# Kernel tuning notes

Measured on AMD Instinct MI355X. Metric: run time of the kernel, lower is better.

Reference implementation:

```python
import jax, jax.numpy as jnp
import numpy as np
import math

D_MODEL, N_HEADS, D_K, D_C, D_HR = 1024, 8, 128, 32, 32
B, S = 4, 2048


def setup_inputs() -> dict:
    key = jax.random.key(0)
    ks = jax.random.split(key, 17)
    def lin(k, fan_in, fan_out):
        lim = 1.0 / math.sqrt(fan_in)
        kw, kb = jax.random.split(k)
        W = jax.random.uniform(kw, (fan_in, fan_out), jnp.float32, -lim, lim)
        b = jax.random.uniform(kb, (fan_out,), jnp.float32, -lim, lim)
        return W, b
    W_DQ, b_DQ = lin(ks[0], D_MODEL, D_C)
    W_UQ, b_UQ = lin(ks[1], D_C, N_HEADS * D_K)
    W_DKV, b_DKV = lin(ks[2], D_MODEL, D_C)
    W_UK, b_UK = lin(ks[3], D_C, N_HEADS * D_K)
    W_UV, b_UV = lin(ks[4], D_C, N_HEADS * D_K)
    W_QR, b_QR = lin(ks[5], D_C, N_HEADS * D_HR)
    W_KR, b_KR = lin(ks[6], D_MODEL, D_HR)
    W_O, b_O = lin(ks[7], N_HEADS * D_K, D_MODEL)
    h_t = jax.random.normal(ks[8], (B, S, D_MODEL), jnp.float32)
    return {"h_t": h_t,
            "W_DQ": W_DQ, "b_DQ": b_DQ, "W_UQ": W_UQ, "b_UQ": b_UQ,
            "W_DKV": W_DKV, "b_DKV": b_DKV, "W_UK": W_UK, "b_UK": b_UK,
            "W_UV": W_UV, "b_UV": b_UV, "W_QR": W_QR, "b_QR": b_QR,
            "W_KR": W_KR, "b_KR": b_KR, "W_O": W_O, "b_O": b_O}


def reference(h_t, W_DQ, b_DQ, W_UQ, b_UQ, W_DKV, b_DKV, W_UK, b_UK,
              W_UV, b_UV, W_QR, b_QR, W_KR, b_KR, W_O, b_O):
    b, s, _ = h_t.shape
    # low-rank latent projections
    c_q = h_t @ W_DQ + b_DQ                       # [B,S,d_c]
    c_kv = h_t @ W_DKV + b_DKV                    # [B,S,d_c]
    # content heads: [B,H,S,d_k]
    q_c = (c_q @ W_UQ + b_UQ).reshape(b, s, N_HEADS, D_K).transpose(0, 2, 1, 3)
    k_c = (c_kv @ W_UK + b_UK).reshape(b, s, N_HEADS, D_K).transpose(0, 2, 1, 3)
    v_c = (c_kv @ W_UV + b_UV).reshape(b, s, N_HEADS, D_K).transpose(0, 2, 1, 3)
    # rope sub-dims (apply_rope is identity in the source): [B,H,S,d_hR]
    q_r = (c_q @ W_QR + b_QR).reshape(b, s, N_HEADS, D_HR).transpose(0, 2, 1, 3)
    k_r = (h_t @ W_KR + b_KR)[:, None, :, :]      # [B,1,S,d_hR], shared across heads
    k_r = jnp.broadcast_to(k_r, (b, N_HEADS, s, D_HR))
    # concat content + rope dims
    q = jnp.concatenate([q_c, q_r], axis=-1)      # [B,H,S,d_k+d_hR]
    k = jnp.concatenate([k_c, k_r], axis=-1)
    scale = 1.0 / math.sqrt(D_K + D_HR)
    scores = jnp.einsum('bhsd,bhtd->bhst', q, k) * scale
    attn = jax.nn.softmax(scores, axis=-1)
    o = jnp.einsum('bhst,bhtd->bhsd', attn, v_c)  # [B,H,S,d_k]
    o = o.transpose(0, 2, 1, 3).reshape(b, s, N_HEADS * D_K)
    return o @ W_O + b_O
```

## Files before the change

kernel.cpp:

```cpp
#include <hip/hip_runtime.h>
#include <hip/hip_bf16.h>

#define B_SZ 4
#define S_SZ 2048
#define DM   1024
#define NH   8
#define DK   128
#define DC   32
#define DHR  32
#define DQK  160
#define T_TOK (B_SZ * S_SZ)
#define SCALE 0.07905694150420949f
#define C2LOG 0.11405506439f
#define NT    (S_SZ / 64)
#define NCOL  3328

typedef unsigned int uint;
typedef unsigned short ushort;
typedef __attribute__((ext_vector_type(8))) short short8;
typedef __attribute__((ext_vector_type(4))) float floatx4;
typedef __attribute__((ext_vector_type(16))) float floatx16;
typedef __attribute__((ext_vector_type(4))) uint uintx4;

__device__ __forceinline__ ushort f2bf(float f) {
    uint u = __float_as_uint(f);
    uint r = u + 0x7fffu + ((u >> 16) & 1u);
    return (ushort)(r >> 16);
}
__device__ __forceinline__ uint packbf(float x, float y) {
    return (uint)f2bf(x) | ((uint)f2bf(y) << 16);
}

__device__ __forceinline__ void glds16(const ushort* g, ushort* l) {
    __builtin_amdgcn_global_load_lds(
        (const __attribute__((address_space(1))) uint*)g,
        (__attribute__((address_space(3))) uint*)l, 16, 0, 0);
}

__global__ __launch_bounds__(256) void prep_kernel(
    const float* __restrict__ W_UQ, const float* __restrict__ b_UQ,
    const float* __restrict__ W_QR, const float* __restrict__ b_QR,
    const float* __restrict__ W_UK, const float* __restrict__ b_UK,
    const float* __restrict__ W_UV, const float* __restrict__ b_UV,
    const float* __restrict__ W_DQ, const float* __restrict__ b_DQ,
    const float* __restrict__ W_DKV, const float* __restrict__ b_DKV,
    const float* __restrict__ W_KR, const float* __restrict__ b_KR,
    ushort* __restrict__ wcat, float* __restrict__ bcat,
    ushort* __restrict__ wdcat, float* __restrict__ bdcat)
{
    __shared__ float t[32][33];
    const int bid = blockIdx.x;
    const int tx = threadIdx.x & 31, ty = threadIdx.x >> 5;

    if (bid < 104) {
        const int c0 = bid * 32;
        const float* W; const float* bias; int stride, sc0;
        if (c0 < 1024)      { W = W_UQ; bias = b_UQ; stride = 1024; sc0 = c0; }
        else if (c0 < 1280) { W = W_QR; bias = b_QR; stride = 256;  sc0 = c0 - 1024; }
        else if (c0 < 2304) { W = W_UK; bias = b_UK; stride = 1024; sc0 = c0 - 1280; }
        else                { W = W_UV; bias = b_UV; stride = 1024; sc0 = c0 - 2304; }
        #pragma unroll
        for (int j = 0; j < 4; ++j) {
            int k = ty + j * 8;
            t[k][tx] = W[(size_t)k * stride + sc0 + tx];
        }
        __syncthreads();
        #pragma unroll
        for (int j = 0; j < 4; ++j) {
            int cc = ty + j * 8;
            wcat[(size_t)(c0 + cc) * 32 + tx] = f2bf(t[tx][cc]);
        }
        if (threadIdx.x < 32) bcat[c0 + threadIdx.x] = bias[sc0 + threadIdx.x];
    } else {
        const int idx = bid - 104;
        const int wsel = idx >> 5;
        const int k0 = (idx & 31) * 32;
        const float* W    = (wsel == 0) ? W_DQ  : (wsel == 1) ? W_DKV : W_KR;
        const float* bias = (wsel == 0) ? b_DQ  : (wsel == 1) ? b_DKV : b_KR;
        #pragma unroll
        for (int j = 0; j < 32; j += 8)
            t[ty + j][tx] = W[(size_t)(k0 + ty + j) * 32 + tx];
        __syncthreads();
        #pragma unroll
        for (int j = 0; j < 32; j += 8)
            wdcat[(size_t)(wsel * 32 + ty + j) * DM + k0 + tx] = f2bf(t[tx][ty + j]);
        if (k0 == 0 && threadIdx.x < 32)
            bdcat[wsel * 32 + threadIdx.x] = bias[threadIdx.x];
    }
}

__global__ __launch_bounds__(256) void wuvo_kernel(
    const float* __restrict__ W_UV, const float* __restrict__ b_UV,
    const float* __restrict__ W_O, const float* __restrict__ b_O,
    ushort* __restrict__ w2t, float* __restrict__ b2)
{
    __shared__ float WO[128][64];
    __shared__ float WUV[32][129];
    const int bid = blockIdx.x;
    if (bid < 128) {
        const int h = bid >> 4, n0 = (bid & 15) * 64;
        for (int idx = threadIdx.x; idx < 8192; idx += 256) {
            int r = idx >> 6, c = idx & 63;
            WO[r][c] = W_O[(size_t)(h * 128 + r) * DM + n0 + c];
        }
        for (int idx = threadIdx.x; idx < 4096; idx += 256) {
            int r = idx >> 7, c = idx & 127;
            WUV[r][c] = W_UV[(size_t)r * DM + h * 128 + c];
        }
        __syncthreads();
        const int i = threadIdx.x & 31, g = threadIdx.x >> 5;
        float acc[8] = {0.f, 0.f, 0.f, 0.f, 0.f, 0.f, 0.f, 0.f};
        for (int j = 0; j < 128; ++j) {
            float wv = WUV[i][j];
            #pragma unroll
            for (int u = 0; u < 8; ++u)
                acc[u] += wv * WO[j][g * 8 + u];
        }
        #pragma unroll
        for (int u = 0; u < 8; ++u)
            w2t[(size_t)(n0 + g * 8 + u) * 256 + h * 32 + i] = f2bf(acc[u]);
    } else {
        const int n = (bid - 128) * 256 + threadIdx.x;
        float acc = b_O[n];
        for (int m = 0; m < 1024; ++m)
            acc += b_UV[m] * W_O[(size_t)m * DM + n];
        b2[n] = acc;
    }
}

__global__ __launch_bounds__(128) void latent_mfma_kernel(
    const float* __restrict__ h_t,
    const ushort* __restrict__ wdcat, const float* __restrict__ bdcat,
    ushort* __restrict__ cqbf, ushort* __restrict__ ckvbf, ushort* __restrict__ krbf)
{
    __shared__ __align__(16) float hsl[2 * 2048];
    const int tid  = threadIdx.x;
    const int wave = tid >> 6;
    const int lane = tid & 63;
    const int quad = lane >> 4;
    const int l16  = lane & 15;
    const int t0 = blockIdx.x * 16;

    int soff[4], ldst[4];
    #pragma unroll
    for (int j = 0; j < 4; ++j) {
        int d = (tid + j * 128) * 16;
        int la = d ^ (((d >> 9) & 7) << 4);
        soff[j] = (d >> 9) * 4096 + (la & 511);
        ldst[j] = (wave * 64 + j * 128) * 16;
    }
    const char* hbase = (const char*)(h_t + (size_t)t0 * DM);

    #pragma unroll
    for (int j = 0; j < 4; ++j)
        glds16((const ushort*)(hbase + soff[j]), (ushort*)((char*)hsl + ldst[j]));

    floatx4 acc[3];
    #pragma unroll
    for (int ct = 0; ct < 3; ++ct) acc[ct] = (floatx4){0.f, 0.f, 0.f, 0.f};

    const int xorm = (l16 & 7) << 4;

    for (int c = 0; c < 8; ++c) {
        const int cur = c & 1, nxt = cur ^ 1;
        __syncthreads();
        if (c + 1 < 8) {
            #pragma unroll
            for (int j = 0; j < 4; ++j)
                glds16((const ushort*)(hbase + (c + 1) * 512 + soff[j]),
                       (ushort*)((char*)hsl + nxt * 8192 + ldst[j]));
        }
        const char* hb = (const char*)hsl + cur * 8192;
        #pragma unroll
        for (int st = 0; st < 4; ++st) {
            const int la0 = l16 * 512 + st * 128 + quad * 32;
            float4 f0 = *(const float4*)(hb + (la0 ^ xorm));
            float4 f1 = *(const float4*)(hb + ((la0 + 16) ^ xorm));
            uint b0, b1, b2x, b3;
            asm("v_cvt_pk_bf16_f32 %0, %1, %2" : "=v"(b0) : "v"(f0.x), "v"(f0.y));
            asm("v_cvt_pk_bf16_f32 %0, %1, %2" : "=v"(b1) : "v"(f0.z), "v"(f0.w));
            asm("v_cvt_pk_bf16_f32 %0, %1, %2" : "=v"(b2x) : "v"(f1.x), "v"(f1.y));
            asm("v_cvt_pk_bf16_f32 %0, %1, %2" : "=v"(b3) : "v"(f1.z), "v"(f1.w));
            short8 bfr = __builtin_bit_cast(short8, (uintx4){b0, b1, b2x, b3});
            #pragma unroll
            for (int ct = 0; ct < 3; ++ct) {
                const int wct = wave * 3 + ct;
                short8 af = *(const short8*)&wdcat[(size_t)(wct * 16 + l16) * DM
                                                   + c * 128 + st * 32 + quad * 8];
                acc[ct] = __builtin_amdgcn_mfma_f32_16x16x32_bf16(af, bfr, acc[ct], 0, 0, 0);
            }
        }
    }

    const int q4 = quad * 4;
    const int tok = t0 + l16;
    #pragma unroll
    for (int ct = 0; ct < 3; ++ct) {
        const int col = (wave * 3 + ct) * 16 + q4;
        float4 b4 = *(const float4*)&bdcat[col];
        uint w0, w1;
        asm("v_cvt_pk_bf16_f32 %0, %1, %2" : "=v"(w0)
            : "v"(acc[ct][0] + b4.x), "v"(acc[ct][1] + b4.y));
        asm("v_cvt_pk_bf16_f32 %0, %1, %2" : "=v"(w1)
            : "v"(acc[ct][2] + b4.z), "v"(acc[ct][3] + b4.w));
        ushort* outp = (col < 32) ? cqbf : (col < 64) ? ckvbf : krbf;
        *(uint2*)&outp[(size_t)tok * 32 + (col & 31)] = make_uint2(w0, w1);
    }
}

__global__ __launch_bounds__(256) void build_qkv_mfma_kernel(
    const ushort* __restrict__ cqbf, const ushort* __restrict__ ckvbf,
    const ushort* __restrict__ krbf,
    const ushort* __restrict__ wcat, const float* __restrict__ bcat,
    ushort* __restrict__ q_ws, ushort* __restrict__ k_ws)
{
    const int tid  = threadIdx.x;
    const int wave = tid >> 6;
    const int lane = tid & 63;
    const int quad = lane >> 4;
    const int l16  = lane & 15;

    const int tok = blockIdx.x * 64 + wave * 16 + l16;
    const int hp  = blockIdx.y;
    const int bb  = tok >> 11, s = tok & 2047;

    const short8 bq  = *(const short8*)&cqbf[tok * 32 + quad * 8];
    const short8 bkv = *(const short8*)&ckvbf[tok * 32 + quad * 8];
    const uint4  kr  = *(const uint4*)&((const uint*)krbf)[tok * 16 + quad * 4];

    const int q4 = quad * 4;

    auto emit = [&](int wrow, ushort* outp, int dbase, short8 bfrag) {
        short8 af = *(const short8*)&wcat[(size_t)(wrow + l16) * 32 + quad * 8];
        floatx4 d = __builtin_amdgcn_mfma_f32_16x16x32_bf16(
            af, bfrag, (floatx4){0.f, 0.f, 0.f, 0.f}, 0, 0, 0);
        float4 b4 = *(const float4*)&bcat[wrow + q4];
        uint w0, w1;
        asm("v_cvt_pk_bf16_f32 %0, %1, %2" : "=v"(w0)
            : "v"(d[0] + b4.x), "v"(d[1] + b4.y));
        asm("v_cvt_pk_bf16_f32 %0, %1, %2" : "=v"(w1)
            : "v"(d[2] + b4.z), "v"(d[3] + b4.w));
        *(uint2*)&outp[dbase + q4] = make_uint2(w0, w1);
    };

    #pragma unroll
    for (int hh = 0; hh < 2; ++hh) {
        const int h = hp * 2 + hh;
        ushort* qp = q_ws + ((size_t)(bb * NH + h) * S_SZ + s) * DQK;
        ushort* kp = k_ws + ((size_t)(bb * NH + h) * S_SZ + s) * DQK;

        #pragma unroll
        for (int seg = 0; seg < 8; ++seg) emit(h * 128 + seg * 16, qp, seg * 16, bq);
        #pragma unroll
        for (int seg = 0; seg < 2; ++seg) emit(1024 + h * 32 + seg * 16, qp, 128 + seg * 16, bq);
        #pragma unroll
        for (int seg = 0; seg < 8; ++seg) emit(1280 + h * 128 + seg * 16, kp, seg * 16, bkv);

        *(uint4*)&kp[128 + quad * 8] = kr;
    }
}

__global__ __launch_bounds__(256, 2) void attn_mfma_kernel(
    const ushort* __restrict__ q_ws, const ushort* __restrict__ k_ws,
    const ushort* __restrict__ ckvbf, ushort* __restrict__ o2)
{
    __shared__ __align__(16) ushort SH[24576];
    const int tid  = threadIdx.x;
    const int wave = tid >> 6;
    const int lane = tid & 63;
    const int l32  = lane & 31;
    const int hi   = lane >> 5;
    const int hi8  = hi * 8;

    const int wg = blockIdx.x;
    const int virt = (wg & 7) * 64 + (wg >> 3);
    const int bh = virt >> 4;
    const int b = bh >> 3, h = bh & 7;
    const int s0 = (virt & 15) * 128;
    const int qrow_base = s0 + wave * 32;

    const ushort* kbase = k_ws + (size_t)bh * S_SZ * DQK;
    const uint* cbase = (const uint*)(ckvbf + (size_t)b * S_SZ * DC);

    int ksrc[5];
    #pragma unroll
    for (int j = 0; j < 5; ++j) {
        int d = (tid + j * 256) * 16;
        int r0 = d / 320;
        int la = d;
        #pragma unroll
        for (int dr = -1; dr <= 1; ++dr) {
            int r = r0 + dr;
            int cand = d ^ ((r & 7) << 4);
            if (cand / 320 == r) la = cand;
        }
        ksrc[j] = la;
    }
    const int kdst_us = (wave * 64) * 8;

    short8 qf[10];
    {
        const ushort* qp = q_ws + ((size_t)bh * S_SZ + qrow_base + l32) * DQK + hi8;
        #pragma unroll
        for (int st = 0; st < 10; ++st)
            qf[st] = *(const short8*)&qp[st * 16];
    }

    floatx16 oa;
    oa = (floatx16){0.f,0.f,0.f,0.f,0.f,0.f,0.f,0.f,
                    0.f,0.f,0.f,0.f,0.f,0.f,0.f,0.f};

    float m2 = -3.0e38f;
    float l_run = 0.f;

    const int kmask = (l32 & 7) << 4;


    {
        #pragma unroll
        for (int j = 0; j < 5; ++j)
            glds16((const ushort*)((const char*)kbase + ksrc[j]),
                   SH + kdst_us + j * 2048);
        if (lane < 16) {
            uint vpa[8], vpb[8];
            #pragma unroll
            for (int c = 0; c < 8; ++c) {
                int kp = wave * 8 + c;
                vpa[c] = cbase[(2 * kp) * 16 + lane];
                vpb[c] = cbase[(2 * kp + 1) * 16 + lane];
            }
            uint lo[8], hh[8];
            #pragma unroll
            for (int c = 0; c < 8; ++c) {
                lo[c] = (vpa[c] & 0xffffu) | (vpb[c] << 16);
                hh[c] = (vpa[c] >> 16) | (vpb[c] & 0xffff0000u);
            }
            char* base = (char*)(SH + 20480);
            const int r0 = 2 * lane, r1 = 2 * lane + 1;
            const int sw0 = (r0 & 7) << 4, sw1 = (r1 & 7) << 4;
            *(uint4*)(base + ((r0 * 128 + wave * 32) ^ sw0))      = make_uint4(lo[0], lo[1], lo[4], lo[5]);
            *(uint4*)(base + ((r0 * 128 + wave * 32 + 16) ^ sw0)) = make_uint4(lo[2], lo[3], lo[6], lo[7]);
            *(uint4*)(base + ((r1 * 128 + wave * 32) ^ sw1))      = make_uint4(hh[0], hh[1], hh[4], hh[5]);
            *(uint4*)(base + ((r1 * 128 + wave * 32 + 16) ^ sw1)) = make_uint4(hh[2], hh[3], hh[6], hh[7]);
        }
    }

    for (int kt = 0; kt < NT; ++kt) {
        const int cur = kt & 1, nxt = cur ^ 1;
        __syncthreads();

        uint vpa[8], vpb[8];
        if (kt + 1 < NT) {
            const char* kg = (const char*)(kbase + (size_t)(kt + 1) * 64 * DQK);
            #pragma unroll
            for (int j = 0; j < 5; ++j)
                glds16((const ushort*)(kg + ksrc[j]),
                       SH + nxt * 10240 + kdst_us + j * 2048);
            if (lane < 16) {
                const uint* cg = cbase + (size_t)(kt + 1) * 64 * 16;
                #pragma unroll
                for (int c = 0; c < 8; ++c) {
                    int kp = wave * 8 + c;
                    vpa[c] = cg[(2 * kp) * 16 + lane];
                    vpb[c] = cg[(2 * kp + 1) * 16 + lane];
                }
            }
        }

        const char* kbufc = (const char*)(SH + cur * 10240);
        floatx16 sc[2];
        __builtin_amdgcn_s_setprio(1);
        #pragma unroll
        for (int kb = 0; kb < 2; ++kb) {
            floatx16 acc = (floatx16){0.f,0.f,0.f,0.f,0.f,0.f,0.f,0.f,
                                      0.f,0.f,0.f,0.f,0.f,0.f,0.f,0.f};
            const int row_la = (kb * 32 + l32) * 320 + hi * 16;
            #pragma unroll
            for (int st = 0; st < 10; ++st) {
                short8 kf = *(const short8*)(kbufc + ((row_la + st * 32) ^ kmask));
                acc = __builtin_amdgcn_mfma_f32_32x32x16_bf16(kf, qf[st], acc, 0, 0, 0);
            }
            sc[kb] = acc;
        }
        __builtin_amdgcn_s_setprio(0);

        {
            float tmax = -3.0e38f;
            #pragma unroll
            for (int kb = 0; kb < 2; ++kb)
                #pragma unroll
                for (int r = 0; r < 16; ++r)
                    tmax = fmaxf(tmax, sc[kb][r]);
            tmax *= C2LOG;
            tmax = fmaxf(tmax, __shfl_xor(tmax, 32));

            if (__any(tmax > m2 + 8.0f)) {
                float mnew = fmaxf(m2, tmax);
                float al = __builtin_amdgcn_exp2f(m2 - mnew);
                m2 = mnew;
                l_run *= al;
                #pragma unroll
                for (int r = 0; r < 16; ++r)
                    oa[r] *= al;
            }

            float rsum = 0.f;
            #pragma unroll
            for (int kb = 0; kb < 2; ++kb)
                #pragma unroll
                for (int r = 0; r < 16; ++r) {
                    float p = __builtin_amdgcn_exp2f(__builtin_fmaf(sc[kb][r], C2LOG, -m2));
                    sc[kb][r] = p;
                    rsum += p;
                }
            rsum += __shfl_xor(rsum, 32);
            l_run += rsum;
        }

        const char* ctc = (const char*)(SH + 20480 + cur * 2048);
        __builtin_amdgcn_s_setprio(1);
        #pragma unroll
        for (int kb = 0; kb < 2; ++kb) {
            #pragma unroll
            for (int s = 0; s < 2; ++s) {
                uint w0, w1, w2, w3;
                asm("v_cvt_pk_bf16_f32 %0, %1, %2" : "=v"(w0)
                    : "v"(sc[kb][8 * s + 0]), "v"(sc[kb][8 * s + 1]));
                asm("v_cvt_pk_bf16_f32 %0, %1, %2" : "=v"(w1)
                    : "v"(sc[kb][8 * s + 2]), "v"(sc[kb][8 * s + 3]));
                asm("v_cvt_pk_bf16_f32 %0, %1, %2" : "=v"(w2)
                    : "v"(sc[kb][8 * s + 4]), "v"(sc[kb][8 * s + 5]));
                asm("v_cvt_pk_bf16_f32 %0, %1, %2" : "=v"(w3)
                    : "v"(sc[kb][8 * s + 6]), "v"(sc[kb][8 * s + 7]));
                short8 pv = __builtin_bit_cast(short8, (uintx4){w0, w1, w2, w3});
                const int la = l32 * 128 + kb * 64 + s * 32 + hi * 16;
                short8 cf = *(const short8*)(ctc + (la ^ kmask));
                oa = __builtin_amdgcn_mfma_f32_32x32x16_bf16(cf, pv, oa, 0, 0, 0);
            }
        }
        __builtin_amdgcn_s_setprio(0);

        if (kt + 1 < NT && lane < 16) {
            uint lo[8], hh[8];
            #pragma unroll
            for (int c = 0; c < 8; ++c) {
                lo[c] = (vpa[c] & 0xffffu) | (vpb[c] << 16);
                hh[c] = (vpa[c] >> 16) | (vpb[c] & 0xffff0000u);
            }
            char* base = (char*)(SH + 20480 + nxt * 2048);
            const int r0 = 2 * lane, r1 = 2 * lane + 1;
            const int sw0 = (r0 & 7) << 4, sw1 = (r1 & 7) << 4;
            *(uint4*)(base + ((r0 * 128 + wave * 32) ^ sw0))      = make_uint4(lo[0], lo[1], lo[4], lo[5]);
            *(uint4*)(base + ((r0 * 128 + wave * 32 + 16) ^ sw0)) = make_uint4(lo[2], lo[3], lo[6], lo[7]);
            *(uint4*)(base + ((r1 * 128 + wave * 32) ^ sw1))      = make_uint4(hh[0], hh[1], hh[4], hh[5]);
            *(uint4*)(base + ((r1 * 128 + wave * 32 + 16) ^ sw1)) = make_uint4(hh[2], hh[3], hh[6], hh[7]);
        }
    }

    {
        float inv = 1.0f / l_run;
        ushort* orow = o2 + ((size_t)(b * S_SZ + qrow_base + l32)) * 256 + h * 32 + hi * 4;
        #pragma unroll
        for (int g = 0; g < 4; ++g) {
            uint w0 = packbf(oa[4 * g + 0] * inv, oa[4 * g + 1] * inv);
            uint w1 = packbf(oa[4 * g + 2] * inv, oa[4 * g + 3] * inv);
            *(uint2*)&orow[g * 8] = make_uint2(w0, w1);
        }
    }
}

__global__ __launch_bounds__(256) void out_gemm_mfma_kernel(
    const ushort* __restrict__ A,
    const ushort* __restrict__ BT,
    const float* __restrict__ b2, float* __restrict__ out)
{
    __shared__ __align__(16) ushort As[128 * 64];
    __shared__ __align__(16) ushort Bs[128 * 64];

    const int tid = threadIdx.x;
    const int wave = tid >> 6;
    const int lane = tid & 63;
    const int quad = lane >> 4;
    const int l16 = lane & 15;
    const int wr = wave >> 1, wc = wave & 1;

    const int wg = blockIdx.x;
    const int virt = (wg & 7) * 64 + (wg >> 3);
    const int n0 = (virt & 7) * 128;
    const int m0 = (virt >> 3) * 128;

    int soff[4], ldst[4];
    #pragma unroll
    for (int j = 0; j < 4; ++j) {
        int d = (tid + j * 256) * 16;
        int la = d ^ (((d >> 7) & 7) << 4);
        soff[j] = (d >> 7) * 512 + (la & 127);
        ldst[j] = (wave * 64 + j * 256) * 16;
    }

    floatx4 acc[4][4];
    #pragma unroll
    for (int mt = 0; mt < 4; ++mt)
        #pragma unroll
        for (int nt = 0; nt < 4; ++nt)
            acc[mt][nt] = (floatx4){0.f, 0.f, 0.f, 0.f};

    const int xorm = (l16 & 7) << 4;

    for (int k0 = 0; k0 < 256; k0 += 64) {
        __syncthreads();
        #pragma unroll
        for (int j = 0; j < 4; ++j) {
            glds16((const ushort*)((const char*)A + (size_t)m0 * 512 + k0 * 2 + soff[j]),
                   (ushort*)((char*)As + ldst[j]));
            glds16((const ushort*)((const char*)BT + (size_t)n0 * 512 + k0 * 2 + soff[j]),
                   (ushort*)((char*)Bs + ldst[j]));
        }
        __syncthreads();

        short8 af[4][2], bf[4][2];
        #pragma unroll
        for (int mt = 0; mt < 4; ++mt)
            #pragma unroll
            for (int hh = 0; hh < 2; ++hh) {
                int la_a = (wr * 64 + mt * 16 + l16) * 128 + hh * 64 + quad * 16;
                af[mt][hh] = *(const short8*)((const char*)As + (la_a ^ xorm));
                int la_b = (wc * 64 + mt * 16 + l16) * 128 + hh * 64 + quad * 16;
                bf[mt][hh] = *(const short8*)((const char*)Bs + (la_b ^ xorm));
            }
        #pragma unroll
        for (int mt = 0; mt < 4; ++mt)
            #pragma unroll
            for (int nt = 0; nt < 4; ++nt) {
                acc[mt][nt] = __builtin_amdgcn_mfma_f32_16x16x32_bf16(af[mt][0], bf[nt][0], acc[mt][nt], 0, 0, 0);
                acc[mt][nt] = __builtin_amdgcn_mfma_f32_16x16x32_bf16(af[mt][1], bf[nt][1], acc[mt][nt], 0, 0, 0);
            }
    }

    float bo[4];
    #pragma unroll
    for (int nt = 0; nt < 4; ++nt) bo[nt] = b2[n0 + wc * 64 + nt * 16 + l16];

    #pragma unroll
    for (int mt = 0; mt < 4; ++mt) {
        #pragma unroll
        for (int r = 0; r < 4; ++r) {
            int row = m0 + wr * 64 + mt * 16 + quad * 4 + r;
            float* orow = out + (size_t)row * DM + n0 + wc * 64;
            #pragma unroll
            for (int nt = 0; nt < 4; ++nt)
                orow[nt * 16 + l16] = acc[mt][nt][r] + bo[nt];
        }
    }
}

extern "C" void kernel_launch(void* const* d_in, const int* in_sizes, int n_in,
                              void* d_out, int out_size, void* d_ws, size_t ws_size,
                              hipStream_t stream) {
    (void)in_sizes; (void)n_in; (void)out_size; (void)ws_size;

    const float* h_t   = (const float*)d_in[0];
    const float* W_DQ  = (const float*)d_in[1];
    const float* b_DQ  = (const float*)d_in[2];
    const float* W_UQ  = (const float*)d_in[3];
    const float* b_UQ  = (const float*)d_in[4];
    const float* W_DKV = (const float*)d_in[5];
    const float* b_DKV = (const float*)d_in[6];
    const float* W_UK  = (const float*)d_in[7];
    const float* b_UK  = (const float*)d_in[8];
    const float* W_UV  = (const float*)d_in[9];
    const float* b_UV  = (const float*)d_in[10];
    const float* W_QR  = (const float*)d_in[11];
    const float* b_QR  = (const float*)d_in[12];
    const float* W_KR  = (const float*)d_in[13];
    const float* b_KR  = (const float*)d_in[14];
    const float* W_O   = (const float*)d_in[15];
    const float* b_O   = (const float*)d_in[16];

    ushort* cqbf  = (ushort*)d_ws;
    ushort* ckvbf = cqbf + (size_t)T_TOK * DC;
    ushort* krbf  = ckvbf + (size_t)T_TOK * DC;
    ushort* wcat  = krbf + (size_t)T_TOK * DC;
    float*  bcat  = (float*)(wcat + (size_t)NCOL * DC);
    ushort* wdcat = (ushort*)(bcat + NCOL);
    float*  bdcat = (float*)(wdcat + (size_t)96 * DM);
    ushort* q_ws  = (ushort*)(bdcat + 96);
    ushort* k_ws  = q_ws + (size_t)B_SZ * NH * S_SZ * DQK;
    ushort* o2    = k_ws + (size_t)B_SZ * NH * S_SZ * DQK;
    ushort* w2t   = o2 + (size_t)T_TOK * 256;
    float*  b2    = (float*)(w2t + (size_t)DM * 256);

    float* out = (float*)d_out;

    prep_kernel<<<200, 256, 0, stream>>>(
        W_UQ, b_UQ, W_QR, b_QR, W_UK, b_UK, W_UV, b_UV,
        W_DQ, b_DQ, W_DKV, b_DKV, W_KR, b_KR,
        wcat, bcat, wdcat, bdcat);

    wuvo_kernel<<<132, 256, 0, stream>>>(
        W_UV, b_UV, W_O, b_O, w2t, b2);

    latent_mfma_kernel<<<T_TOK / 16, 128, 0, stream>>>(
        h_t, wdcat, bdcat, cqbf, ckvbf, krbf);

    build_qkv_mfma_kernel<<<dim3(T_TOK / 64, 4), 256, 0, stream>>>(
        cqbf, ckvbf, krbf, wcat, bcat, q_ws, k_ws);

    attn_mfma_kernel<<<512, 256, 0, stream>>>(
        q_ws, k_ws, ckvbf, o2);

    out_gemm_mfma_kernel<<<512, 256, 0, stream>>>(
        o2, w2t, b2, out);
}
```

Measured before the change: 262.1 us.

## Absorb W_UK into query projection so attention runs on 64-dim latent keys

Folds W_UQ·W_UKᵀ (and b_UQ·W_UKᵀ) into a per-head 32x32 weight, so each head's query becomes a 64-wide vector (32 latent plus 32 rope). Keys are read directly as the shared [c_kv, k_r] latent, which removes materialising the per-head 160-dim K and Q tensors. QK^T drops from 10 MFMA steps to 4 and LDS use shrinks. The two weight-prep kernels are merged into one launch. Dropping b_UK is valid because it adds a per-row constant that softmax cancels, but folding weights into bf16 changes rounding.

```diff
diff --git a/kernel.cpp b/kernel.cpp
--- a/kernel.cpp
+++ b/kernel.cpp
@@ -13,7 +13,6 @@
 #define SCALE 0.07905694150420949f
 #define C2LOG 0.11405506439f
 #define NT    (S_SZ / 64)
-#define NCOL  3328
 
 typedef unsigned int uint;
 typedef unsigned short ushort;
@@ -37,7 +36,7 @@
         (__attribute__((address_space(3))) uint*)l, 16, 0, 0);
 }
 
-__global__ __launch_bounds__(256) void prep_kernel(
+__global__ __launch_bounds__(256) void prep2_kernel(
     const float* __restrict__ W_UQ, const float* __restrict__ b_UQ,
     const float* __restrict__ W_QR, const float* __restrict__ b_QR,
     const float* __restrict__ W_UK, const float* __restrict__ b_UK,
@@ -45,70 +44,30 @@
     const float* __restrict__ W_DQ, const float* __restrict__ b_DQ,
     const float* __restrict__ W_DKV, const float* __restrict__ b_DKV,
     const float* __restrict__ W_KR, const float* __restrict__ b_KR,
-    ushort* __restrict__ wcat, float* __restrict__ bcat,
-    ushort* __restrict__ wdcat, float* __restrict__ bdcat)
-{
-    __shared__ float t[32][33];
-    const int bid = blockIdx.x;
-    const int tx = threadIdx.x & 31, ty = threadIdx.x >> 5;
-
-    if (bid < 104) {
-        const int c0 = bid * 32;
-        const float* W; const float* bias; int stride, sc0;
-        if (c0 < 1024)      { W = W_UQ; bias = b_UQ; stride = 1024; sc0 = c0; }
-        else if (c0 < 1280) { W = W_QR; bias = b_QR; stride = 256;  sc0 = c0 - 1024; }
-        else if (c0 < 2304) { W = W_UK; bias = b_UK; stride = 1024; sc0 = c0 - 1280; }
-        else                { W = W_UV; bias = b_UV; stride = 1024; sc0 = c0 - 2304; }
-        #pragma unroll
-        for (int j = 0; j < 4; ++j) {
-            int k = ty + j * 8;
-            t[k][tx] = W[(size_t)k * stride + sc0 + tx];
-        }
-        __syncthreads();
-        #pragma unroll
-        for (int j = 0; j < 4; ++j) {
-            int cc = ty + j * 8;
-            wcat[(size_t)(c0 + cc) * 32 + tx] = f2bf(t[tx][cc]);
-        }
-        if (threadIdx.x < 32) bcat[c0 + threadIdx.x] = bias[sc0 + threadIdx.x];
-    } else {
-        const int idx = bid - 104;
-        const int wsel = idx >> 5;
-        const int k0 = (idx & 31) * 32;
-        const float* W    = (wsel == 0) ? W_DQ  : (wsel == 1) ? W_DKV : W_KR;
-        const float* bias = (wsel == 0) ? b_DQ  : (wsel == 1) ? b_DKV : b_KR;
-        #pragma unroll
-        for (int j = 0; j < 32; j += 8)
-            t[ty + j][tx] = W[(size_t)(k0 + ty + j) * 32 + tx];
-        __syncthreads();
-        #pragma unroll
-        for (int j = 0; j < 32; j += 8)
-            wdcat[(size_t)(wsel * 32 + ty + j) * DM + k0 + tx] = f2bf(t[tx][ty + j]);
-        if (k0 == 0 && threadIdx.x < 32)
-            bdcat[wsel * 32 + threadIdx.x] = bias[threadIdx.x];
-    }
-}
-
-__global__ __launch_bounds__(256) void wuvo_kernel(
-    const float* __restrict__ W_UV, const float* __restrict__ b_UV,
     const float* __restrict__ W_O, const float* __restrict__ b_O,
+    ushort* __restrict__ wdcat, float* __restrict__ bdcat,
+    ushort* __restrict__ wq2cat, float* __restrict__ bq2cat,
     ushort* __restrict__ w2t, float* __restrict__ b2)
 {
-    __shared__ float WO[128][64];
-    __shared__ float WUV[32][129];
+    __shared__ float S1[128 * 64];
+    __shared__ float S2[32 * 129];
     const int bid = blockIdx.x;
+    const int tid = threadIdx.x;
+
     if (bid < 128) {
+        float (*WO)[64] = (float(*)[64])S1;
+        float (*WUV)[129] = (float(*)[129])S2;
         const int h = bid >> 4, n0 = (bid & 15) * 64;
-        for (int idx = threadIdx.x; idx < 8192; idx += 256) {
+        for (int idx = tid; idx < 8192; idx += 256) {
             int r = idx >> 6, c = idx & 63;
             WO[r][c] = W_O[(size_t)(h * 128 + r) * DM + n0 + c];
         }
-        for (int idx = threadIdx.x; idx < 4096; idx += 256) {
+        for (int idx = tid; idx < 4096; idx += 256) {
             int r = idx >> 7, c = idx & 127;
             WUV[r][c] = W_UV[(size_t)r * DM + h * 128 + c];
         }
         __syncthreads();
-        const int i = threadIdx.x & 31, g = threadIdx.x >> 5;
+        const int i = tid & 31, g = tid >> 5;
         float acc[8] = {0.f, 0.f, 0.f, 0.f, 0.f, 0.f, 0.f, 0.f};
         for (int j = 0; j < 128; ++j) {
             float wv = WUV[i][j];
@@ -119,19 +78,71 @@
         #pragma unroll
         for (int u = 0; u < 8; ++u)
             w2t[(size_t)(n0 + g * 8 + u) * 256 + h * 32 + i] = f2bf(acc[u]);
-    } else {
-        const int n = (bid - 128) * 256 + threadIdx.x;
+    } else if (bid < 132) {
+        const int n = (bid - 128) * 256 + tid;
         float acc = b_O[n];
         for (int m = 0; m < 1024; ++m)
             acc += b_UV[m] * W_O[(size_t)m * DM + n];
         b2[n] = acc;
+    } else if (bid < 140) {
+        const int h = bid - 132;
+        float (*UQ)[128] = (float(*)[128])S1;
+        float (*UK)[128] = (float(*)[128])S2;
+        for (int idx = tid; idx < 4096; idx += 256) {
+            int r = idx >> 7, c = idx & 127;
+            UQ[r][c] = W_UQ[(size_t)r * DM + h * 128 + c];
+            UK[r][c] = W_UK[(size_t)r * DM + h * 128 + c];
+        }
+        __syncthreads();
+        const int j = tid & 31, g = tid >> 5;
+        float acc[4] = {0.f, 0.f, 0.f, 0.f};
+        for (int d = 0; d < 128; ++d) {
+            float uk = UK[j][d];
+            #pragma unroll
+            for (int u = 0; u < 4; ++u)
+                acc[u] += UQ[g * 4 + u][d] * uk;
+        }
+        #pragma unroll
+        for (int u = 0; u < 4; ++u)
+            wq2cat[(size_t)(h * 64 + j) * 32 + g * 4 + u] = f2bf(acc[u]);
+        if (tid < 32) {
+            float a = 0.f;
+            for (int d = 0; d < 128; ++d)
+                a += b_UQ[h * 128 + d] * UK[tid][d];
+            bq2cat[h * 64 + tid] = a;
+        }
+        {
+            const int jr = tid >> 3, i0 = (tid & 7) * 4;
+            #pragma unroll
+            for (int u = 0; u < 4; ++u)
+                wq2cat[(size_t)(h * 64 + 32 + jr) * 32 + i0 + u] =
+                    f2bf(W_QR[(size_t)(i0 + u) * 256 + h * 32 + jr]);
+            if (tid < 32) bq2cat[h * 64 + 32 + tid] = b_QR[h * 32 + tid];
+        }
+    } else {
+        float (*t33)[33] = (float(*)[33])S2;
+        const int idx = bid - 140;
+        const int wsel = idx >> 5;
+        const int k0 = (idx & 31) * 32;
+        const int tx = tid & 31, ty = tid >> 5;
+        const float* W    = (wsel == 0) ? W_DQ  : (wsel == 1) ? W_DKV : W_KR;
+        const float* bias = (wsel == 0) ? b_DQ  : (wsel == 1) ? b_DKV : b_KR;
+        #pragma unroll
+        for (int j = 0; j < 32; j += 8)
+            t33[ty + j][tx] = W[(size_t)(k0 + ty + j) * 32 + tx];
+        __syncthreads();
+        #pragma unroll
+        for (int j = 0; j < 32; j += 8)
+            wdcat[(size_t)(wsel * 32 + ty + j) * DM + k0 + tx] = f2bf(t33[tx][ty + j]);
+        if (k0 == 0 && tid < 32)
+            bdcat[wsel * 32 + tid] = bias[tid];
     }
 }
 
 __global__ __launch_bounds__(128) void latent_mfma_kernel(
     const float* __restrict__ h_t,
     const ushort* __restrict__ wdcat, const float* __restrict__ bdcat,
-    ushort* __restrict__ cqbf, ushort* __restrict__ ckvbf, ushort* __restrict__ krbf)
+    ushort* __restrict__ cqbf, ushort* __restrict__ kv2)
 {
     __shared__ __align__(16) float hsl[2 * 2048];
     const int tid  = threadIdx.x;
@@ -203,16 +214,17 @@
             : "v"(acc[ct][0] + b4.x), "v"(acc[ct][1] + b4.y));
         asm("v_cvt_pk_bf16_f32 %0, %1, %2" : "=v"(w1)
             : "v"(acc[ct][2] + b4.z), "v"(acc[ct][3] + b4.w));
-        ushort* outp = (col < 32) ? cqbf : (col < 64) ? ckvbf : krbf;
-        *(uint2*)&outp[(size_t)tok * 32 + (col & 31)] = make_uint2(w0, w1);
-    }
-}
-
-__global__ __launch_bounds__(256) void build_qkv_mfma_kernel(
-    const ushort* __restrict__ cqbf, const ushort* __restrict__ ckvbf,
-    const ushort* __restrict__ krbf,
-    const ushort* __restrict__ wcat, const float* __restrict__ bcat,
-    ushort* __restrict__ q_ws, ushort* __restrict__ k_ws)
+        if (col < 32)
+            *(uint2*)&cqbf[(size_t)tok * 32 + col] = make_uint2(w0, w1);
+        else
+            *(uint2*)&kv2[(size_t)tok * 64 + (col - 32)] = make_uint2(w0, w1);
+    }
+}
+
+__global__ __launch_bounds__(256) void build_q2_kernel(
+    const ushort* __restrict__ cqbf,
+    const ushort* __restrict__ wq2cat, const float* __restrict__ bq2cat,
+    ushort* __restrict__ q2_ws)
 {
     const int tid  = threadIdx.x;
     const int wave = tid >> 6;
@@ -221,50 +233,33 @@
     const int l16  = lane & 15;
 
     const int tok = blockIdx.x * 64 + wave * 16 + l16;
-    const int hp  = blockIdx.y;
-    const int bb  = tok >> 11, s = tok & 2047;
-
-    const short8 bq  = *(const short8*)&cqbf[tok * 32 + quad * 8];
-    const short8 bkv = *(const short8*)&ckvbf[tok * 32 + quad * 8];
-    const uint4  kr  = *(const uint4*)&((const uint*)krbf)[tok * 16 + quad * 4];
-
+    const int c0  = blockIdx.y * 256;
+
+    const short8 bq = *(const short8*)&cqbf[(size_t)tok * 32 + quad * 8];
     const int q4 = quad * 4;
-
-    auto emit = [&](int wrow, ushort* outp, int dbase, short8 bfrag) {
-        short8 af = *(const short8*)&wcat[(size_t)(wrow + l16) * 32 + quad * 8];
+    ushort* orow = q2_ws + (size_t)tok * 512;
+
+    #pragma unroll
+    for (int seg = 0; seg < 16; ++seg) {
+        const int wrow = c0 + seg * 16;
+        short8 af = *(const short8*)&wq2cat[(size_t)(wrow + l16) * 32 + quad * 8];
         floatx4 d = __builtin_amdgcn_mfma_f32_16x16x32_bf16(
-            af, bfrag, (floatx4){0.f, 0.f, 0.f, 0.f}, 0, 0, 0);
-        float4 b4 = *(const float4*)&bcat[wrow + q4];
+            af, bq, (floatx4){0.f, 0.f, 0.f, 0.f}, 0, 0, 0);
+        float4 b4 = *(const float4*)&bq2cat[wrow + q4];
         uint w0, w1;
         asm("v_cvt_pk_bf16_f32 %0, %1, %2" : "=v"(w0)
             : "v"(d[0] + b4.x), "v"(d[1] + b4.y));
         asm("v_cvt_pk_bf16_f32 %0, %1, %2" : "=v"(w1)
             : "v"(d[2] + b4.z), "v"(d[3] + b4.w));
-        *(uint2*)&outp[dbase + q4] = make_uint2(w0, w1);
-    };
-
-    #pragma unroll
-    for (int hh = 0; hh < 2; ++hh) {
-        const int h = hp * 2 + hh;
-        ushort* qp = q_ws + ((size_t)(bb * NH + h) * S_SZ + s) * DQK;
-        ushort* kp = k_ws + ((size_t)(bb * NH + h) * S_SZ + s) * DQK;
-
-        #pragma unroll
-        for (int seg = 0; seg < 8; ++seg) emit(h * 128 + seg * 16, qp, seg * 16, bq);
-        #pragma unroll
-        for (int seg = 0; seg < 2; ++seg) emit(1024 + h * 32 + seg * 16, qp, 128 + seg * 16, bq);
-        #pragma unroll
-        for (int seg = 0; seg < 8; ++seg) emit(1280 + h * 128 + seg * 16, kp, seg * 16, bkv);
-
-        *(uint4*)&kp[128 + quad * 8] = kr;
+        *(uint2*)&orow[wrow + q4] = make_uint2(w0, w1);
     }
 }
 
 __global__ __launch_bounds__(256, 2) void attn_mfma_kernel(
-    const ushort* __restrict__ q_ws, const ushort* __restrict__ k_ws,
-    const ushort* __restrict__ ckvbf, ushort* __restrict__ o2)
+    const ushort* __restrict__ q2_ws, const ushort* __restrict__ kv2,
+    ushort* __restrict__ o2)
 {
-    __shared__ __align__(16) ushort SH[24576];
+    __shared__ __align__(16) ushort SH[12288];
     const int tid  = threadIdx.x;
     const int wave = tid >> 6;
     const int lane = tid & 63;
@@ -279,30 +274,22 @@
     const int s0 = (virt & 15) * 128;
     const int qrow_base = s0 + wave * 32;
 
-    const ushort* kbase = k_ws + (size_t)bh * S_SZ * DQK;
-    const uint* cbase = (const uint*)(ckvbf + (size_t)b * S_SZ * DC);
-
-    int ksrc[5];
-    #pragma unroll
-    for (int j = 0; j < 5; ++j) {
+    const char* kvbase = (const char*)(kv2 + (size_t)b * S_SZ * 64);
+
+    int ksrc[2], kldst[2];
+    #pragma unroll
+    for (int j = 0; j < 2; ++j) {
         int d = (tid + j * 256) * 16;
-        int r0 = d / 320;
-        int la = d;
-        #pragma unroll
-        for (int dr = -1; dr <= 1; ++dr) {
-            int r = r0 + dr;
-            int cand = d ^ ((r & 7) << 4);
-            if (cand / 320 == r) la = cand;
-        }
-        ksrc[j] = la;
-    }
-    const int kdst_us = (wave * 64) * 8;
-
-    short8 qf[10];
+        ksrc[j] = d ^ (((d >> 7) & 7) << 4);
+        kldst[j] = (wave * 64 + j * 256) * 8;
+    }
+
+    short8 qf[4];
     {
-        const ushort* qp = q_ws + ((size_t)bh * S_SZ + qrow_base + l32) * DQK + hi8;
-        #pragma unroll
-        for (int st = 0; st < 10; ++st)
+        const ushort* qp = q2_ws + ((size_t)(b * S_SZ) + qrow_base + l32) * 512
+                         + h * 64 + hi8;
+        #pragma unroll
+        for (int st = 0; st < 4; ++st)
             qf[st] = *(const short8*)&qp[st * 16];
     }
 
@@ -315,19 +302,18 @@
 
     const int kmask = (l32 & 7) << 4;
 
-
     {
         #pragma unroll
-        for (int j = 0; j < 5; ++j)
-            glds16((const ushort*)((const char*)kbase + ksrc[j]),
-                   SH + kdst_us + j * 2048);
+        for (int j = 0; j < 2; ++j)
+            glds16((const ushort*)(kvbase + ksrc[j]), SH + kldst[j]);
         if (lane < 16) {
+            const uint* cg = (const uint*)kvbase;
             uint vpa[8], vpb[8];
             #pragma unroll
             for (int c = 0; c < 8; ++c) {
                 int kp = wave * 8 + c;
-                vpa[c] = cbase[(2 * kp) * 16 + lane];
-                vpb[c] = cbase[(2 * kp + 1) * 16 + lane];
+                vpa[c] = cg[(2 * kp) * 32 + lane];
+                vpb[c] = cg[(2 * kp + 1) * 32 + lane];
             }
             uint lo[8], hh[8];
             #pragma unroll
@@ -335,7 +321,7 @@
                 lo[c] = (vpa[c] & 0xffffu) | (vpb[c] << 16);
                 hh[c] = (vpa[c] >> 16) | (vpb[c] & 0xffff0000u);
             }
-            char* base = (char*)(SH + 20480);
+            char* base = (char*)(SH + 8192);
             const int r0 = 2 * lane, r1 = 2 * lane + 1;
             const int sw0 = (r0 & 7) << 4, sw1 = (r1 & 7) << 4;
             *(uint4*)(base + ((r0 * 128 + wave * 32) ^ sw0))      = make_uint4(lo[0], lo[1], lo[4], lo[5]);
@@ -351,32 +337,31 @@
 
         uint vpa[8], vpb[8];
         if (kt + 1 < NT) {
-            const char* kg = (const char*)(kbase + (size_t)(kt + 1) * 64 * DQK);
-            #pragma unroll
-            for (int j = 0; j < 5; ++j)
-                glds16((const ushort*)(kg + ksrc[j]),
-                       SH + nxt * 10240 + kdst_us + j * 2048);
+            const char* kg = kvbase + (size_t)(kt + 1) * 8192;
+            #pragma unroll
+            for (int j = 0; j < 2; ++j)
+                glds16((const ushort*)(kg + ksrc[j]), SH + nxt * 4096 + kldst[j]);
             if (lane < 16) {
-                const uint* cg = cbase + (size_t)(kt + 1) * 64 * 16;
+                const uint* cg = (const uint*)kg;
                 #pragma unroll
                 for (int c = 0; c < 8; ++c) {
                     int kp = wave * 8 + c;
-                    vpa[c] = cg[(2 * kp) * 16 + lane];
-                    vpb[c] = cg[(2 * kp + 1) * 16 + lane];
+                    vpa[c] = cg[(2 * kp) * 32 + lane];
+                    vpb[c] = cg[(2 * kp + 1) * 32 + lane];
                 }
             }
         }
 
-        const char* kbufc = (const char*)(SH + cur * 10240);
+        const char* kbufc = (const char*)(SH + cur * 4096);
         floatx16 sc[2];
         __builtin_amdgcn_s_setprio(1);
         #pragma unroll
         for (int kb = 0; kb < 2; ++kb) {
             floatx16 acc = (floatx16){0.f,0.f,0.f,0.f,0.f,0.f,0.f,0.f,
                                       0.f,0.f,0.f,0.f,0.f,0.f,0.f,0.f};
-            const int row_la = (kb * 32 + l32) * 320 + hi * 16;
-            #pragma unroll
-            for (int st = 0; st < 10; ++st) {
+            const int row_la = (kb * 32 + l32) * 128 + hi * 16;
+            #pragma unroll
+            for (int st = 0; st < 4; ++st) {
                 short8 kf = *(const short8*)(kbufc + ((row_la + st * 32) ^ kmask));
                 acc = __builtin_amdgcn_mfma_f32_32x32x16_bf16(kf, qf[st], acc, 0, 0, 0);
             }
@@ -417,7 +402,7 @@
             l_run += rsum;
         }
 
-        const char* ctc = (const char*)(SH + 20480 + cur * 2048);
+        const char* ctc = (const char*)(SH + 8192 + cur * 2048);
         __builtin_amdgcn_s_setprio(1);
         #pragma unroll
         for (int kb = 0; kb < 2; ++kb) {
@@ -447,7 +432,7 @@
                 lo[c] = (vpa[c] & 0xffffu) | (vpb[c] << 16);
                 hh[c] = (vpa[c] >> 16) | (vpb[c] & 0xffff0000u);
             }
-            char* base = (char*)(SH + 20480 + nxt * 2048);
+            char* base = (char*)(SH + 8192 + nxt * 2048);
             const int r0 = 2 * lane, r1 = 2 * lane + 1;
             const int sw0 = (r0 & 7) << 4, sw1 = (r1 & 7) << 4;
             *(uint4*)(base + ((r0 * 128 + wave * 32) ^ sw0))      = make_uint4(lo[0], lo[1], lo[4], lo[5]);
@@ -576,38 +561,34 @@
     const float* b_KR  = (const float*)d_in[14];
     const float* W_O   = (const float*)d_in[15];
     const float* b_O   = (const float*)d_in[16];
-
-    ushort* cqbf  = (ushort*)d_ws;
-    ushort* ckvbf = cqbf + (size_t)T_TOK * DC;
-    ushort* krbf  = ckvbf + (size_t)T_TOK * DC;
-    ushort* wcat  = krbf + (size_t)T_TOK * DC;
-    float*  bcat  = (float*)(wcat + (size_t)NCOL * DC);
-    ushort* wdcat = (ushort*)(bcat + NCOL);
-    float*  bdcat = (float*)(wdcat + (size_t)96 * DM);
-    ushort* q_ws  = (ushort*)(bdcat + 96);
-    ushort* k_ws  = q_ws + (size_t)B_SZ * NH * S_SZ * DQK;
-    ushort* o2    = k_ws + (size_t)B_SZ * NH * S_SZ * DQK;
-    ushort* w2t   = o2 + (size_t)T_TOK * 256;
-    float*  b2    = (float*)(w2t + (size_t)DM * 256);
+    (void)b_UK;
+
+    ushort* cqbf   = (ushort*)d_ws;
+    ushort* kv2    = cqbf + (size_t)T_TOK * DC;
+    ushort* wdcat  = kv2 + (size_t)T_TOK * 64;
+    float*  bdcat  = (float*)(wdcat + (size_t)96 * DM);
+    ushort* wq2cat = (ushort*)(bdcat + 96);
+    float*  bq2cat = (float*)(wq2cat + (size_t)512 * 32);
+    ushort* q2_ws  = (ushort*)(bq2cat + 512);
+    ushort* o2     = q2_ws + (size_t)T_TOK * 512;
+    ushort* w2t    = o2 + (size_t)T_TOK * 256;
+    float*  b2     = (float*)(w2t + (size_t)DM * 256);
 
     float* out = (float*)d_out;
 
-    prep_kernel<<<200, 256, 0, stream>>>(
+    prep2_kernel<<<236, 256, 0, stream>>>(
         W_UQ, b_UQ, W_QR, b_QR, W_UK, b_UK, W_UV, b_UV,
-        W_DQ, b_DQ, W_DKV, b_DKV, W_KR, b_KR,
-        wcat, bcat, wdcat, bdcat);
-
-    wuvo_kernel<<<132, 256, 0, stream>>>(
-        W_UV, b_UV, W_O, b_O, w2t, b2);
+        W_DQ, b_DQ, W_DKV, b_DKV, W_KR, b_KR, W_O, b_O,
+        wdcat, bdcat, wq2cat, bq2cat, w2t, b2);
 
     latent_mfma_kernel<<<T_TOK / 16, 128, 0, stream>>>(
-        h_t, wdcat, bdcat, cqbf, ckvbf, krbf);
-
-    build_qkv_mfma_kernel<<<dim3(T_TOK / 64, 4), 256, 0, stream>>>(
-        cqbf, ckvbf, krbf, wcat, bcat, q_ws, k_ws);
+        h_t, wdcat, bdcat, cqbf, kv2);
+
+    build_q2_kernel<<<dim3(T_TOK / 64, 2), 256, 0, stream>>>(
+        cqbf, wq2cat, bq2cat, q2_ws);
 
     attn_mfma_kernel<<<512, 256, 0, stream>>>(
-        q_ws, k_ws, ckvbf, o2);
+        q2_ws, kv2, o2);
 
     out_gemm_mfma_kernel<<<512, 256, 0, stream>>>(
         o2, w2t, b2, out);
```

Result: faster. 228.9 us (-12.7%).
